# Kernel optimization log

Measured on AMD Instinct MI355X. Metric: run time of the kernel, lower is better.

## Reference

```python
import jax, jax.numpy as jnp
import numpy as np

N, M = 100000, 800000
F_IN, F_E, H = 64, 16, 64
T_NODE, T_EDGE = 2, 3
HEAD_DIM = 16.0


def setup_inputs() -> dict:
    key = jax.random.key(0)
    ks = jax.random.split(key, 16)
    inp = {
        "x": jax.random.normal(ks[0], (N, F_IN), jnp.float32),
        "edge_feat": jax.random.normal(ks[1], (M, F_E), jnp.float32),
        "node_type": jax.random.randint(ks[2], (N,), 0, T_NODE, jnp.int32),
        "edge_src": jax.random.randint(ks[3], (M,), 0, N, jnp.int32),
        "edge_dst": jax.random.randint(ks[4], (M,), 0, N, jnp.int32),
        "edge_type": jax.random.randint(ks[5], (M,), 0, T_EDGE, jnp.int32),
    }
    s_n = 1.0 / np.sqrt(F_IN)
    s_e = 1.0 / np.sqrt(F_E)
    for i, name in enumerate(["W1", "W2", "W3", "W4"]):
        inp[name] = jax.random.normal(ks[6 + i], (T_NODE, F_IN, H), jnp.float32) * s_n
        inp["b" + name[1]] = jax.random.normal(ks[10 + i], (T_NODE, H), jnp.float32) * 0.01
    inp["W5"] = jax.random.normal(ks[14], (T_EDGE, F_E, H), jnp.float32) * s_e
    inp["b5"] = jax.random.normal(ks[15], (T_EDGE, H), jnp.float32) * 0.01
    return inp


def _node_proj(x, W, b, node_type):
    # per-node-type linear: [T,F,H] weights, select row per node type
    p = jnp.einsum('nf,tfh->tnh', x, W) + b[:, None, :]      # [T,N,H]
    return jnp.take_along_axis(p, node_type[None, :, None], axis=0)[0]  # [N,H]


def reference(x, edge_feat, W1, b1, W2, b2, W3, b3, W4, b4, W5, b5,
              node_type, edge_src, edge_dst, edge_type):
    n = x.shape[0]
    h1 = _node_proj(x, W1, b1, node_type)
    h2 = _node_proj(x, W2, b2, node_type)
    h3 = _node_proj(x, W3, b3, node_type)
    h4 = _node_proj(x, W4, b4, node_type)
    # per-edge-type linear via weight gather (F_E is small)
    w5e = jnp.einsum('mf,mfh->mh', edge_feat, W5[edge_type]) + b5[edge_type]  # [M,H]
    # scalar attention logit per edge (w3_i . (w4_j + w5_ij)) / sqrt(head_dim)
    num = jnp.sum(h3[edge_dst] * (h4[edge_src] + w5e), axis=-1)  # [M]
    # softmax over a single scalar per edge == 1.0 exactly (faithful to source)
    score = jax.nn.softmax((num / jnp.sqrt(HEAD_DIM))[:, None], axis=-1)[:, 0]  # [M]
    msg = score[:, None] * (h2[edge_src] + w5e)                  # [M,H]
    out = h1 + jax.ops.segment_sum(msg, edge_dst, num_segments=n)
    return out
```

## Files before the change

### kernel.cpp

```cpp
#include <hip/hip_runtime.h>


#define CAP 16
#define OVF_CAP 32768

typedef __attribute__((ext_vector_type(8))) short short8;
typedef __attribute__((ext_vector_type(4))) float f32x4;

__device__ __forceinline__ float b2f(unsigned short u) {
    union { unsigned v; float f; } x; x.v = ((unsigned)u) << 16; return x.f;
}
__device__ __forceinline__ unsigned short f2b(float f) {
    union { float f; unsigned v; } x; x.f = f;
    unsigned u = x.v;
    unsigned r = (u + 0x7FFFu + ((u >> 16) & 1u)) >> 16;
    return (unsigned short)r;
}

__global__ __launch_bounds__(256) void k0_init(
    int* __restrict__ zeroBase, int nZero,
    const float* __restrict__ W1, const float* __restrict__ W2,
    const float* __restrict__ W5, const float* __restrict__ b5,
    unsigned short* __restrict__ wtb, unsigned short* __restrict__ wtb5)
{
    int idx = blockIdx.x * 256 + threadIdx.x;
    if (idx < nZero) zeroBase[idx] = 0;
    if (idx < 16384) {
        int mm = idx >> 12;
        int r  = idx & 4095;
        int n  = r >> 6;
        int k  = r & 63;
        const float* src = ((mm < 2) ? W1 : W2) + (mm & 1) * 4096;
        wtb[mm * 4096 + n * 64 + k] = f2b(src[k * 64 + n]);
    }
    if (idx < 4096) {
        int h = idx >> 6;
        int j = idx & 63;
        float wv = 0.f;
        if (j < 48)      wv = W5[j * 64 + h];
        else if (j < 51) wv = b5[(j - 48) * 64 + h];
        wtb5[h * 64 + j] = f2b(wv);
    }
}

__global__ __launch_bounds__(256) void k1_fused(
    const float* __restrict__ x, const int* __restrict__ nt,
    const unsigned short* __restrict__ wtb,
    const float* __restrict__ b1, const float* __restrict__ b2,
    const int* __restrict__ esrc, const int* __restrict__ edst,
    const int* __restrict__ etype,
    int* __restrict__ cnt32, int* __restrict__ ovfCnt,
    int4* __restrict__ ovf, int2* __restrict__ rec,
    unsigned short* __restrict__ h1b, unsigned short* __restrict__ h2b,
    int N, int M)
{
    __shared__ __align__(16) unsigned short sx[128 * 72];
    __shared__ int snt[128];

    int tid = threadIdx.x;

    if (blockIdx.x & 1) {
        int e0 = (blockIdx.x >> 1) * 1024 + tid;
        int dd[4], ssrc[4], tty[4];
        bool v[4];
#pragma unroll
        for (int j = 0; j < 4; ++j) {
            int e = e0 + j * 256;
            v[j] = e < M;
            int ec = v[j] ? e : 0;
            dd[j]   = edst[ec];
            ssrc[j] = esrc[ec];
            tty[j]  = etype[ec];
        }
        int pos[4];
#pragma unroll
        for (int j = 0; j < 4; ++j)
            if (v[j]) pos[j] = atomicAdd(&cnt32[dd[j]], 1);
#pragma unroll
        for (int j = 0; j < 4; ++j) {
            if (!v[j]) continue;
            int packed = ssrc[j] | (tty[j] << 20);
            int e = e0 + j * 256;
            if (pos[j] < CAP) {
                rec[dd[j] * CAP + pos[j]] = make_int2(packed, e);
            } else {
                int slot = atomicAdd(ovfCnt, 1);
                if (slot < OVF_CAP) ovf[slot] = make_int4(packed, e, dd[j], 0);
            }
        }
        return;
    }

    int rowbase = (blockIdx.x >> 1) * 128;

    if (tid < 128) {
        int r = rowbase + tid;
        snt[tid] = (r < N) ? nt[r] : 0;
    }

    int fr = (tid & 15) * 4;
    int ir = tid >> 4;
#pragma unroll
    for (int it = 0; it < 8; ++it) {
        int i = it * 16 + ir;
        int r = rowbase + i;
        float4 v = make_float4(0.f, 0.f, 0.f, 0.f);
        if (r < N) v = *(const float4*)&x[(size_t)r * 64 + fr];
        ushort4 p;
        p.x = f2b(v.x); p.y = f2b(v.y); p.z = f2b(v.z); p.w = f2b(v.w);
        *(ushort4*)&sx[i * 72 + fr] = p;
    }
    __syncthreads();

    int lane = tid & 63;
    int wid  = tid >> 6;
    int q    = lane >> 4;
    int cc   = lane & 15;
    int m0   = wid * 32;

    f32x4 acc[4][2][4];
#pragma unroll
    for (int mm = 0; mm < 4; ++mm)
#pragma unroll
        for (int s = 0; s < 2; ++s)
#pragma unroll
            for (int t = 0; t < 4; ++t)
                acc[mm][s][t] = (f32x4){0.f, 0.f, 0.f, 0.f};

#pragma unroll
    for (int k0 = 0; k0 < 64; k0 += 32) {
        int ko = k0 + q * 8;
        short8 af0 = *(short8*)&sx[(m0 + cc) * 72 + ko];
        short8 af1 = *(short8*)&sx[(m0 + 16 + cc) * 72 + ko];
#pragma unroll
        for (int mm = 0; mm < 4; ++mm)
#pragma unroll
            for (int t = 0; t < 4; ++t) {
                short8 bf = *(const short8*)
                    &wtb[mm * 4096 + (t * 16 + cc) * 64 + ko];
                acc[mm][0][t] = __builtin_amdgcn_mfma_f32_16x16x32_bf16(
                    af0, bf, acc[mm][0][t], 0, 0, 0);
                acc[mm][1][t] = __builtin_amdgcn_mfma_f32_16x16x32_bf16(
                    af1, bf, acc[mm][1][t], 0, 0, 0);
            }
    }

    float b1v[2][4], b2v[2][4];
#pragma unroll
    for (int ty = 0; ty < 2; ++ty)
#pragma unroll
        for (int t = 0; t < 4; ++t) {
            b1v[ty][t] = b1[ty * 64 + t * 16 + cc];
            b2v[ty][t] = b2[ty * 64 + t * 16 + cc];
        }

#pragma unroll
    for (int s = 0; s < 2; ++s)
#pragma unroll
        for (int reg = 0; reg < 4; ++reg) {
            int rl_ = m0 + s * 16 + q * 4 + reg;
            int r = rowbase + rl_;
            if (r < N) {
                int ty = snt[rl_];
#pragma unroll
                for (int t = 0; t < 4; ++t) {
                    float v1 = (ty ? acc[1][s][t][reg] : acc[0][s][t][reg])
                               + b1v[ty][t];
                    float v2 = (ty ? acc[3][s][t][reg] : acc[2][s][t][reg])
                               + b2v[ty][t];
                    h1b[(size_t)r * 64 + t * 16 + cc] = f2b(v1);
                    h2b[(size_t)r * 64 + t * 16 + cc] = f2b(v2);
                }
            }
        }
}

__global__ __launch_bounds__(256) void k2_gather_mm(
    const float* __restrict__ ef, const int2* __restrict__ rec,
    const int* __restrict__ cnt32,
    const float* __restrict__ W5, const float* __restrict__ b5,
    const unsigned short* __restrict__ wtb5,
    const int4* __restrict__ ovf, const int* __restrict__ ovfCnt,
    const unsigned short* __restrict__ h1b,
    const unsigned short* __restrict__ h2b, float* __restrict__ out,
    int N, int gatherBlocks, int ovfBlocks)
{
    __shared__ __align__(16) unsigned short sa[32 * 136];
    __shared__ __align__(16) unsigned short sHb[32 * 66];
    __shared__ int sCnt[32];

    int tid = threadIdx.x;
    int lane = tid & 63;
    int wid = tid >> 6;

    if (blockIdx.x >= (unsigned)gatherBlocks) {
        int novf = min(*ovfCnt, OVF_CAP);
        int gw = (blockIdx.x - gatherBlocks) * 4 + wid;
        int nw = ovfBlocks * 4;
        for (int ri = gw; ri < novf; ri += nw) {
            int4 o = ovf[ri];
            int s = o.x & 0xFFFFF;
            int t = (unsigned)o.x >> 20;
            float acc = b5[t * 64 + lane] + b2f(h2b[((size_t)s << 6) | lane]);
#pragma unroll
            for (int f = 0; f < 16; ++f)
                acc = fmaf(ef[(size_t)o.y * 16 + f],
                           W5[(t * 16 + f) * 64 + lane], acc);
            unsafeAtomicAdd(&out[(size_t)o.z * 64 + lane], acc);
        }
        return;
    }

    {
        ushort4 z; z.x = 0; z.y = 0; z.z = 0; z.w = 0;
        if (tid < 192) {
            int row = tid / 6;
            int w6 = tid - row * 6;
            int sp = (w6 < 3) ? (52 + w6 * 4) : (116 + (w6 - 3) * 4);
            *(ushort4*)&sa[row * 136 + sp] = z;
        }
    }

    int myt = (lane < 48) ? (lane >> 4) : (lane - 48);
    unsigned myf = lane & 15;
    bool fl = lane < 48;
    int wbase = blockIdx.x * 32 + wid * 8;

    int cnts[8];
#pragma unroll
    for (int g = 0; g < 8; ++g) {
        int d = wbase + g;
        cnts[g] = (d < N) ? cnt32[d] : 0;
    }
    if (lane == 0) {
#pragma unroll
        for (int g = 0; g < 8; ++g) sCnt[wid * 8 + g] = cnts[g];
    }

#pragma unroll 1
    for (int gp = 0; gp < 8; gp += 2) {
        int dA = wbase + gp, dB = dA + 1;
        int dgA = min(cnts[gp], CAP);
        int dgB = min(cnts[gp + 1], CAP);
        unsigned baseA = (unsigned)(dA < N ? dA : 0) * CAP;
        unsigned baseB = (unsigned)(dB < N ? dB : 0) * CAP;

        int2 rA[8], rB[8];
#pragma unroll
        for (int j = 0; j < 8; ++j) rA[j] = rec[baseA + j];
#pragma unroll
        for (int j = 0; j < 8; ++j) rB[j] = rec[baseB + j];

        float hvA[8], evA[8], hvB[8], evB[8];
#pragma unroll
        for (int j = 0; j < 8; ++j) {
            bool ok = j < dgA;
            unsigned s = ok ? ((unsigned)rA[j].x & 0xFFFFFu) : 0u;
            unsigned e = ok ? (unsigned)rA[j].y : 0u;
            hvA[j] = b2f(h2b[((size_t)s << 6) | (unsigned)lane]);
            evA[j] = ef[(e << 4) | myf];
        }
#pragma unroll
        for (int j = 0; j < 8; ++j) {
            bool ok = j < dgB;
            unsigned s = ok ? ((unsigned)rB[j].x & 0xFFFFFu) : 0u;
            unsigned e = ok ? (unsigned)rB[j].y : 0u;
            hvB[j] = b2f(h2b[((size_t)s << 6) | (unsigned)lane]);
            evB[j] = ef[(e << 4) | myf];
        }

        float accHA = 0.f, accSA = 0.f, accHB = 0.f, accSB = 0.f;
#pragma unroll
        for (int j = 0; j < 8; ++j) {
            bool okA = j < dgA;
            int tA = (int)((unsigned)rA[j].x >> 20);
            accHA += okA ? hvA[j] : 0.f;
            float vA = fl ? evA[j] : 1.0f;
            accSA += (okA && tA == myt) ? vA : 0.f;
            bool okB = j < dgB;
            int tB = (int)((unsigned)rB[j].x >> 20);
            accHB += okB ? hvB[j] : 0.f;
            float vB = fl ? evB[j] : 1.0f;
            accSB += (okB && tB == myt) ? vB : 0.f;
        }

        if (dgA > 8) {
            int2 r2[8];
#pragma unroll
            for (int j = 0; j < 8; ++j)
                r2[j] = rec[baseA + (unsigned)min(8 + j, dgA - 1)];
#pragma unroll
            for (int j = 0; j < 8; ++j) {
                unsigned s = (unsigned)r2[j].x & 0xFFFFFu;
                float hv = b2f(h2b[((size_t)s << 6) | (unsigned)lane]);
                float evv = ef[((unsigned)r2[j].y << 4) | myf];
                int t = (int)((unsigned)r2[j].x >> 20);
                bool ok = (8 + j) < dgA;
                accHA += ok ? hv : 0.f;
                float v = fl ? evv : 1.0f;
                accSA += (ok && t == myt) ? v : 0.f;
            }
        }
        if (dgB > 8) {
            int2 r2[8];
#pragma unroll
            for (int j = 0; j < 8; ++j)
                r2[j] = rec[baseB + (unsigned)min(8 + j, dgB - 1)];
#pragma unroll
            for (int j = 0; j < 8; ++j) {
                unsigned s = (unsigned)r2[j].x & 0xFFFFFu;
                float hv = b2f(h2b[((size_t)s << 6) | (unsigned)lane]);
                float evv = ef[((unsigned)r2[j].y << 4) | myf];
                int t = (int)((unsigned)r2[j].x >> 20);
                bool ok = (8 + j) < dgB;
                accHB += ok ? hv : 0.f;
                float v = fl ? evv : 1.0f;
                accSB += (ok && t == myt) ? v : 0.f;
            }
        }

        int wdA = wid * 8 + gp, wdB = wdA + 1;
        if (lane < 52) {
            unsigned short hiA = f2b(accSA);
            sa[wdA * 136 + lane] = hiA;
            sa[wdA * 136 + 64 + lane] = f2b(accSA - b2f(hiA));
            unsigned short hiB = f2b(accSB);
            sa[wdB * 136 + lane] = hiB;
            sa[wdB * 136 + 64 + lane] = f2b(accSB - b2f(hiB));
        }
        sHb[wdA * 66 + lane] = f2b(accHA);
        sHb[wdB * 66 + lane] = f2b(accHB);
    }
    __syncthreads();

    int q  = lane >> 4;
    int cc = lane & 15;
    int s  = wid & 1;
    int t0 = wid >> 1;

    float h1v[4][2];
#pragma unroll
    for (int reg = 0; reg < 4; ++reg) {
        int rl = s * 16 + q * 4 + reg;
        int d = blockIdx.x * 32 + rl;
        unsigned dc = (unsigned)((d < N) ? d : 0);
        h1v[reg][0] = b2f(h1b[(size_t)dc * 64 + t0 * 16 + cc]);
        h1v[reg][1] = b2f(h1b[(size_t)dc * 64 + (t0 + 2) * 16 + cc]);
    }

    f32x4 acc0 = (f32x4){0.f, 0.f, 0.f, 0.f};
    f32x4 acc1 = (f32x4){0.f, 0.f, 0.f, 0.f};
#pragma unroll
    for (int k0 = 0; k0 < 128; k0 += 32) {
        int ko = k0 + q * 8;
        int kb = ko & 63;
        short8 af = *(short8*)&sa[(s * 16 + cc) * 136 + ko];
        short8 bf0 = *(const short8*)&wtb5[(t0 * 16 + cc) * 64 + kb];
        short8 bf1 = *(const short8*)&wtb5[((t0 + 2) * 16 + cc) * 64 + kb];
        acc0 = __builtin_amdgcn_mfma_f32_16x16x32_bf16(af, bf0, acc0, 0, 0, 0);
        acc1 = __builtin_amdgcn_mfma_f32_16x16x32_bf16(af, bf1, acc1, 0, 0, 0);
    }

#pragma unroll
    for (int reg = 0; reg < 4; ++reg) {
        int rl = s * 16 + q * 4 + reg;
        int d = blockIdx.x * 32 + rl;
        if (d < N) {
            int c0 = t0 * 16 + cc;
            int c1 = (t0 + 2) * 16 + cc;
            float v0 = acc0[reg] + b2f(sHb[rl * 66 + c0]) + h1v[reg][0];
            float v1 = acc1[reg] + b2f(sHb[rl * 66 + c1]) + h1v[reg][1];
            float* p0 = &out[(size_t)d * 64 + c0];
            float* p1 = &out[(size_t)d * 64 + c1];
            if (sCnt[rl] > CAP) {
                unsafeAtomicAdd(p0, v0);
                unsafeAtomicAdd(p1, v1);
            } else {
                *p0 = v0;
                *p1 = v1;
            }
        }
    }
}

extern "C" void kernel_launch(void* const* d_in, const int* in_sizes, int n_in,
                              void* d_out, int out_size, void* d_ws, size_t ws_size,
                              hipStream_t stream) {
    const float* x  = (const float*)d_in[0];
    const float* ef = (const float*)d_in[1];
    const int* nt   = (const int*)d_in[2];
    const int* es   = (const int*)d_in[3];
    const int* ed   = (const int*)d_in[4];
    const int* et   = (const int*)d_in[5];
    const float* W1 = (const float*)d_in[6];
    const float* b1 = (const float*)d_in[7];
    const float* W2 = (const float*)d_in[8];
    const float* b2 = (const float*)d_in[9];
    const float* W5 = (const float*)d_in[14];
    const float* b5 = (const float*)d_in[15];

    int N = in_sizes[2];
    int M = in_sizes[3];

    char* w = (char*)d_ws;
    size_t off = 0;
    unsigned short* h2b = (unsigned short*)(w + off); off += (size_t)N * 64 * 2;
    off = (off + 255) & ~(size_t)255;
    unsigned short* h1b = (unsigned short*)(w + off); off += (size_t)N * 64 * 2;
    off = (off + 255) & ~(size_t)255;
    int2* rec = (int2*)(w + off); off += (size_t)N * CAP * 8;
    off = (off + 255) & ~(size_t)255;
    int4* ovf = (int4*)(w + off); off += (size_t)OVF_CAP * 16;
    off = (off + 255) & ~(size_t)255;
    unsigned short* wtb = (unsigned short*)(w + off); off += 4 * 4096 * 2;
    off = (off + 255) & ~(size_t)255;
    unsigned short* wtb5 = (unsigned short*)(w + off); off += 64 * 64 * 2;
    off = (off + 255) & ~(size_t)255;
    int* ovfCnt = (int*)(w + off);
    int* cnt32  = (int*)(w + off + 64);
    int nZero = 16 + N;

    float* out = (float*)d_out;

    int initBlocks = (nZero + 255) / 256;
    k0_init<<<initBlocks, 256, 0, stream>>>(
        ovfCnt, nZero, W1, W2, W5, b5, wtb, wtb5);

    int gemmBlocks    = (N + 127) / 128;
    int scatterBlocks = (M + 1023) / 1024;
    int gb1 = 2 * max(gemmBlocks, scatterBlocks);
    k1_fused<<<gb1, 256, 0, stream>>>(
        x, nt, wtb, b1, b2, es, ed, et,
        cnt32, ovfCnt, ovf, rec, h1b, h2b, N, M);

    int gatherBlocks = (N + 31) / 32;
    int ovfBlocks = 32;
    k2_gather_mm<<<gatherBlocks + ovfBlocks, 256, 0, stream>>>(
        ef, rec, cnt32, W5, b5, wtb5, ovf, ovfCnt, h1b, h2b, out,
        N, gatherBlocks, ovfBlocks);
}
```

Measured before the change: 275.6 us.

## Make each wave own 16 destination rows end-to-end, dropping block barrier

The gather+MFMA kernel now gives each wave 16 destination nodes and has it run the MFMA epilogue over all four output column tiles for those rows, so rows no longer cross waves. That removes the __syncthreads between the gather and matrix phases, and the shared count array is replaced by re-reading cnt32 from global memory. Each block now covers 64 nodes with twice the LDS (about 26 KB), which halves the block count and may lower occupancy. Each wave also does twice the serial gather iterations and issues more B-fragment loads per wave.

New measurement: 278.0 us. Within noise of the previous version (+0.9%).

```diff
diff --git a/kernel.cpp b/kernel.cpp
--- a/kernel.cpp
+++ b/kernel.cpp
@@ -185,9 +185,8 @@
     const unsigned short* __restrict__ h2b, float* __restrict__ out,
     int N, int gatherBlocks, int ovfBlocks)
 {
-    __shared__ __align__(16) unsigned short sa[32 * 136];
-    __shared__ __align__(16) unsigned short sHb[32 * 66];
-    __shared__ int sCnt[32];
+    __shared__ __align__(16) unsigned short sa[64 * 136];
+    __shared__ __align__(16) unsigned short sHb[64 * 66];
 
     int tid = threadIdx.x;
     int lane = tid & 63;
@@ -213,32 +212,32 @@
 
     {
         ushort4 z; z.x = 0; z.y = 0; z.z = 0; z.w = 0;
-        if (tid < 192) {
-            int row = tid / 6;
-            int w6 = tid - row * 6;
-            int sp = (w6 < 3) ? (52 + w6 * 4) : (116 + (w6 - 3) * 4);
-            *(ushort4*)&sa[row * 136 + sp] = z;
+#pragma unroll
+        for (int k = 0; k < 2; ++k) {
+            int idx = lane + k * 64;
+            if (idx < 96) {
+                int row = idx / 6;
+                int w6 = idx - row * 6;
+                int sp = (w6 < 3) ? (52 + w6 * 4) : (116 + (w6 - 3) * 4);
+                *(ushort4*)&sa[(wid * 16 + row) * 136 + sp] = z;
+            }
         }
     }
 
     int myt = (lane < 48) ? (lane >> 4) : (lane - 48);
     unsigned myf = lane & 15;
     bool fl = lane < 48;
-    int wbase = blockIdx.x * 32 + wid * 8;
-
-    int cnts[8];
-#pragma unroll
-    for (int g = 0; g < 8; ++g) {
+    int wbase = blockIdx.x * 64 + wid * 16;
+
+    int cnts[16];
+#pragma unroll
+    for (int g = 0; g < 16; ++g) {
         int d = wbase + g;
         cnts[g] = (d < N) ? cnt32[d] : 0;
     }
-    if (lane == 0) {
-#pragma unroll
-        for (int g = 0; g < 8; ++g) sCnt[wid * 8 + g] = cnts[g];
-    }
 
 #pragma unroll 1
-    for (int gp = 0; gp < 8; gp += 2) {
+    for (int gp = 0; gp < 16; gp += 2) {
         int dA = wbase + gp, dB = dA + 1;
         int dgA = min(cnts[gp], CAP);
         int dgB = min(cnts[gp + 1], CAP);
@@ -319,7 +318,7 @@
             }
         }
 
-        int wdA = wid * 8 + gp, wdB = wdA + 1;
+        int wdA = wid * 16 + gp, wdB = wdA + 1;
         if (lane < 52) {
             unsigned short hiA = f2b(accSA);
             sa[wdA * 136 + lane] = hiA;
@@ -331,53 +330,53 @@
         sHb[wdA * 66 + lane] = f2b(accHA);
         sHb[wdB * 66 + lane] = f2b(accHB);
     }
-    __syncthreads();
 
     int q  = lane >> 4;
     int cc = lane & 15;
-    int s  = wid & 1;
-    int t0 = wid >> 1;
-
-    float h1v[4][2];
+    int rowb = wid * 16;
+
+    float h1v[4][4];
+    int cq[4];
 #pragma unroll
     for (int reg = 0; reg < 4; ++reg) {
-        int rl = s * 16 + q * 4 + reg;
-        int d = blockIdx.x * 32 + rl;
+        int d = wbase + q * 4 + reg;
         unsigned dc = (unsigned)((d < N) ? d : 0);
-        h1v[reg][0] = b2f(h1b[(size_t)dc * 64 + t0 * 16 + cc]);
-        h1v[reg][1] = b2f(h1b[(size_t)dc * 64 + (t0 + 2) * 16 + cc]);
-    }
-
-    f32x4 acc0 = (f32x4){0.f, 0.f, 0.f, 0.f};
-    f32x4 acc1 = (f32x4){0.f, 0.f, 0.f, 0.f};
+        cq[reg] = cnt32[dc];
+#pragma unroll
+        for (int t = 0; t < 4; ++t)
+            h1v[reg][t] = b2f(h1b[(size_t)dc * 64 + t * 16 + cc]);
+    }
+
+    f32x4 acc[4];
+#pragma unroll
+    for (int t = 0; t < 4; ++t) acc[t] = (f32x4){0.f, 0.f, 0.f, 0.f};
 #pragma unroll
     for (int k0 = 0; k0 < 128; k0 += 32) {
         int ko = k0 + q * 8;
         int kb = ko & 63;
-        short8 af = *(short8*)&sa[(s * 16 + cc) * 136 + ko];
-        short8 bf0 = *(const short8*)&wtb5[(t0 * 16 + cc) * 64 + kb];
-        short8 bf1 = *(const short8*)&wtb5[((t0 + 2) * 16 + cc) * 64 + kb];
-        acc0 = __builtin_amdgcn_mfma_f32_16x16x32_bf16(af, bf0, acc0, 0, 0, 0);
-        acc1 = __builtin_amdgcn_mfma_f32_16x16x32_bf16(af, bf1, acc1, 0, 0, 0);
+        short8 af = *(short8*)&sa[(rowb + cc) * 136 + ko];
+#pragma unroll
+        for (int t = 0; t < 4; ++t) {
+            short8 bf = *(const short8*)&wtb5[(t * 16 + cc) * 64 + kb];
+            acc[t] = __builtin_amdgcn_mfma_f32_16x16x32_bf16(
+                af, bf, acc[t], 0, 0, 0);
+        }
     }
 
 #pragma unroll
     for (int reg = 0; reg < 4; ++reg) {
-        int rl = s * 16 + q * 4 + reg;
-        int d = blockIdx.x * 32 + rl;
+        int rl = q * 4 + reg;
+        int d = wbase + rl;
         if (d < N) {
-            int c0 = t0 * 16 + cc;
-            int c1 = (t0 + 2) * 16 + cc;
-            float v0 = acc0[reg] + b2f(sHb[rl * 66 + c0]) + h1v[reg][0];
-            float v1 = acc1[reg] + b2f(sHb[rl * 66 + c1]) + h1v[reg][1];
-            float* p0 = &out[(size_t)d * 64 + c0];
-            float* p1 = &out[(size_t)d * 64 + c1];
-            if (sCnt[rl] > CAP) {
-                unsafeAtomicAdd(p0, v0);
-                unsafeAtomicAdd(p1, v1);
-            } else {
-                *p0 = v0;
-                *p1 = v1;
+            bool atom = cq[reg] > CAP;
+#pragma unroll
+            for (int t = 0; t < 4; ++t) {
+                int c = t * 16 + cc;
+                float v = acc[t][reg] + b2f(sHb[(rowb + rl) * 66 + c])
+                        + h1v[reg][t];
+                float* p = &out[(size_t)d * 64 + c];
+                if (atom) unsafeAtomicAdd(p, v);
+                else      *p = v;
             }
         }
     }
@@ -433,7 +432,7 @@
         x, nt, wtb, b1, b2, es, ed, et,
         cnt32, ovfCnt, ovf, rec, h1b, h2b, N, M);
 
-    int gatherBlocks = (N + 31) / 32;
+    int gatherBlocks = (N + 63) / 64;
     int ovfBlocks = 32;
     k2_gather_mm<<<gatherBlocks + ovfBlocks, 256, 0, stream>>>(
         ef, rec, cnt32, W5, b5, wtb5, ovf, ovfCnt, h1b, h2b, out,
```
